# Kernel tuning notes

Hardware: AMD Instinct MI355X
Metric: run time of the kernel (lower is better)

Reference implementation:

```python
import jax, jax.numpy as jnp
import numpy as np

T, B, D_IN, D_H = 256, 256, 1024, 1024


def setup_inputs() -> dict:
    key = jax.random.key(0)
    k1, k2 = jax.random.split(key)
    seq = jax.random.normal(k1, (T, B, D_IN), dtype=jnp.float32)
    # Kaiming-ish init so tanh does not saturate
    W = jax.random.normal(k2, (D_H, D_IN + D_H), dtype=jnp.float32) / np.sqrt(D_IN + D_H)
    b = jnp.zeros((D_H,), dtype=jnp.float32)
    return {"seq": seq, "W": W, "b": b}


def reference(seq, W, b):
    # seq: (T, B, d_in); W: (d_h, d_in + d_h); b: (d_h,)
    d_h = W.shape[0]
    h0 = jnp.zeros((seq.shape[1], d_h), dtype=seq.dtype)

    def step(h, x):
        # h_{t+1} = tanh(W [h_t ; x_t] + b)
        h_new = jnp.tanh(jnp.concatenate([h, x], axis=-1) @ W.T + b)
        return h_new, h_new

    _, hs = jax.lax.scan(step, h0, seq)  # hs: (T, B, d_h)
    # Original returns the full hidden-state history including the initial zero state
    return jnp.concatenate([h0[None], hs], axis=0)  # (T+1, B, d_h)
```

## Files before the change

kernel.cpp:

```cpp
#include <hip/hip_runtime.h>

#define T_STEPS 256
#define BATCH   256
#define DIN     1024
#define DH      1024

typedef _Float16 half8_t __attribute__((ext_vector_type(8)));
typedef _Float16 half4_t __attribute__((ext_vector_type(4)));
typedef float    f32x4_t __attribute__((ext_vector_type(4)));

#define LDH  1032
#define LGW  72
#define LDS_BYTES 36864

#define CPOL_SYS 17

union H4U { half4_t h; unsigned long long u; };
union HU  { _Float16 h; unsigned short u; };

__device__ __forceinline__ float ftanh(float x) {
    float t = x * 2.885390081777927f;
    float e = exp2f(t);
    float r = __builtin_amdgcn_rcpf(e + 1.0f);
    return 1.0f - 2.0f * r;
}

__global__ __launch_bounds__(256) void cvt_w(const float* __restrict__ W,
                                             _Float16* __restrict__ Wh,
                                             _Float16* __restrict__ Wx) {
    const int part = blockIdx.x >> 9;
    size_t base = ((size_t)(blockIdx.x & 511) * 256 + threadIdx.x) * 8;
    const int n = (int)(base >> 10);
    const int k = (int)(base & 1023);
    const float4* s = reinterpret_cast<const float4*>(W + (size_t)n * 2048 + part * 1024 + k);
    float4 a = s[0], b = s[1];
    half8_t h;
    h[0] = (_Float16)a.x; h[1] = (_Float16)a.y;
    h[2] = (_Float16)a.z; h[3] = (_Float16)a.w;
    h[4] = (_Float16)b.x; h[5] = (_Float16)b.y;
    h[6] = (_Float16)b.z; h[7] = (_Float16)b.w;
    _Float16* dst = part ? Wx : Wh;
    *reinterpret_cast<half8_t*>(dst + base) = h;
}

__global__ __launch_bounds__(256) void zero_h0(float* __restrict__ out,
                                               int* __restrict__ flags,
                                               int* __restrict__ zrdy) {
    size_t i = (size_t)blockIdx.x * 256 + threadIdx.x;
    reinterpret_cast<float4*>(out)[i] = make_float4(0.f, 0.f, 0.f, 0.f);
    if (blockIdx.x == 0) {
#pragma unroll
        for (int j = 0; j < 16; ++j)
            __hip_atomic_store(&flags[(int)threadIdx.x * 16 + j], 0,
                               __ATOMIC_RELAXED, __HIP_MEMORY_SCOPE_SYSTEM);
    } else if (blockIdx.x == 1) {
#pragma unroll
        for (int j = 0; j < 16; ++j)
            __hip_atomic_store(&zrdy[(int)threadIdx.x * 16 + j], 0,
                               __ATOMIC_RELAXED, __HIP_MEMORY_SCOPE_SYSTEM);
    }
}

__global__ __launch_bounds__(256, 1) void fused_pipeline(
        const _Float16* __restrict__ Wh,
        const _Float16* __restrict__ Wx,
        const float* __restrict__ bias,
        const float* __restrict__ seq,
        _Float16* __restrict__ Hh,
        int* __restrict__ flags,
        int* __restrict__ zrdy,
        float* __restrict__ out) {
    __shared__ __align__(16) char ldsraw[LDS_BYTES];
    const int tid = threadIdx.x;
    const int bid = blockIdx.x;

    const int wave = tid >> 6;
    const int lane = tid & 63;
    const int fr   = lane & 15;
    const int quad = lane >> 4;

    if (bid >= 256) {
        _Float16* la = reinterpret_cast<_Float16*>(ldsraw);
        _Float16* lb = la + 128 * LGW;

        const int id   = bid - 256;
        const int nblk = (id >> 3) & 7;
        const int mblk = (id & 7) + 8 * (id >> 6);
        const int m0 = mblk * 128;
        const int n0 = nblk * 128;

        const float* __restrict__ X = seq + (size_t)m0 * 1024;
        float* __restrict__ Z = out + (size_t)BATCH * DH + (size_t)m0 * 1024 + n0;

        const int ar = tid >> 1;
        const int kh = tid & 1;
        const float*    Asrc = X  + (size_t)ar * 1024 + kh * 32;
        const _Float16* Bsrc = Wx + (size_t)(n0 + ar) * 1024 + kh * 32;

        float4 af[8];
        uint4  bq[4];
        auto load_tiles = [&](int kb) {
            const float4* s4 = reinterpret_cast<const float4*>(Asrc + kb);
#pragma unroll
            for (int i = 0; i < 8; ++i) af[i] = s4[i];
            const uint4* sb = reinterpret_cast<const uint4*>(Bsrc + kb);
#pragma unroll
            for (int i = 0; i < 4; ++i) bq[i] = sb[i];
        };
        auto store_tiles = [&]() {
#pragma unroll
            for (int j = 0; j < 4; ++j) {
                half8_t h;
                h[0] = (_Float16)af[2 * j].x;     h[1] = (_Float16)af[2 * j].y;
                h[2] = (_Float16)af[2 * j].z;     h[3] = (_Float16)af[2 * j].w;
                h[4] = (_Float16)af[2 * j + 1].x; h[5] = (_Float16)af[2 * j + 1].y;
                h[6] = (_Float16)af[2 * j + 1].z; h[7] = (_Float16)af[2 * j + 1].w;
                *reinterpret_cast<half8_t*>(&la[ar * LGW + kh * 32 + j * 8]) = h;
            }
#pragma unroll
            for (int i = 0; i < 4; ++i)
                *reinterpret_cast<uint4*>(&lb[ar * LGW + kh * 32 + i * 8]) = bq[i];
        };

        const int wm = (wave >> 1) * 64;
        const int wn = (wave & 1) * 64;

        f32x4_t acc[4][4];
#pragma unroll
        for (int i = 0; i < 4; ++i)
#pragma unroll
            for (int j = 0; j < 4; ++j) acc[i][j] = (f32x4_t){0.f, 0.f, 0.f, 0.f};

        load_tiles(0);
#pragma unroll 1
        for (int it = 0; it < 16; ++it) {
            store_tiles();
            __syncthreads();
            if (it < 15) load_tiles((it + 1) * 64);
#pragma unroll
            for (int kk = 0; kk < 2; ++kk) {
                const int ko = kk * 32 + quad * 8;
                half8_t a[4], b[4];
#pragma unroll
                for (int mi = 0; mi < 4; ++mi)
                    a[mi] = *reinterpret_cast<const half8_t*>(
                        &la[(wm + mi * 16 + fr) * LGW + ko]);
#pragma unroll
                for (int ni = 0; ni < 4; ++ni)
                    b[ni] = *reinterpret_cast<const half8_t*>(
                        &lb[(wn + ni * 16 + fr) * LGW + ko]);
#pragma unroll
                for (int mi = 0; mi < 4; ++mi)
#pragma unroll
                    for (int ni = 0; ni < 4; ++ni)
                        acc[mi][ni] = __builtin_amdgcn_mfma_f32_16x16x32_f16(
                            a[mi], b[ni], acc[mi][ni], 0, 0, 0);
            }
            __syncthreads();
        }

        {
            float* S = reinterpret_cast<float*>(ldsraw) + wave * (16 * 20);
#pragma unroll
            for (int ni = 0; ni < 4; ++ni) {
                const float bv = bias[n0 + wn + ni * 16 + fr];
#pragma unroll
                for (int mi = 0; mi < 4; ++mi) {
#pragma unroll
                    for (int q = 0; q < 4; ++q)
                        S[(quad * 4 + q) * 20 + fr] = acc[mi][ni][q] + bv;
                    f32x4_t t = *reinterpret_cast<const f32x4_t*>(
                        &S[fr * 20 + quad * 4]);
                    float* dst = &Z[(size_t)(wm + mi * 16 + fr) * 1024
                                    + wn + ni * 16 + quad * 4];
                    asm volatile("global_store_dwordx4 %0, %1, off sc0 sc1"
                                 :: "v"(dst), "v"(t) : "memory");
                }
            }
        }
        asm volatile("s_waitcnt vmcnt(0)" ::: "memory");
        __syncthreads();
        if (tid == 0)
            __hip_atomic_store(&zrdy[mblk * 8 + nblk], 1,
                               __ATOMIC_RELAXED, __HIP_MEMORY_SCOPE_SYSTEM);
        return;
    }

    _Float16* hL = reinterpret_cast<_Float16*>(ldsraw);

    const int m = bid & 15;
    const int n = bid >> 4;

    half8_t bfrag[32];
    {
        const _Float16* wp = Wh + (size_t)(n * 64 + wave * 16 + fr) * DH + quad * 8;
#pragma unroll
        for (int ks = 0; ks < 32; ++ks)
            bfrag[ks] = *reinterpret_cast<const half8_t*>(wp + ks * 32);
    }

    const int r  = tid >> 4;
    const int c4 = (tid & 15) * 4;
    int* myflag = flags + (m * 16 + n) * 16;
    const int zcol  = n >> 1;
    const int mhalf = m >> 3;

    const int ecol = n * 64 + wave * 16 + fr;
    const int erow0 = m * 16 + quad * 4;

    {
        if (tid == 0) {
            const int* zf = zrdy + (0 + mhalf) * 8 + zcol;
            int g = 0;
            while (!__hip_atomic_load(zf, __ATOMIC_RELAXED,
                                      __HIP_MEMORY_SCOPE_SYSTEM)) {
                if (++g > (1 << 25)) break;
            }
        }
        __syncthreads();

        float* o1 = out + ((size_t)BATCH + (size_t)(m * 16 + r)) * DH + n * 64 + c4;
        float zv[4];
#pragma unroll
        for (int j = 0; j < 4; ++j)
            zv[j] = __hip_atomic_load(o1 + j, __ATOMIC_RELAXED,
                                      __HIP_MEMORY_SCOPE_SYSTEM);
        float4 v = make_float4(ftanh(zv[0]), ftanh(zv[1]),
                               ftanh(zv[2]), ftanh(zv[3]));
        *reinterpret_cast<float4*>(o1) = v;
        H4U cv;
        cv.h[0] = (_Float16)v.x; cv.h[1] = (_Float16)v.y;
        cv.h[2] = (_Float16)v.z; cv.h[3] = (_Float16)v.w;
        __hip_atomic_store(
            (unsigned long long*)(Hh + ((size_t)BATCH + (size_t)(m * 16 + r)) * DH
                                  + n * 64 + c4),
            cv.u, __ATOMIC_RELAXED, __HIP_MEMORY_SCOPE_SYSTEM);
        __syncthreads();
        if (tid == 0)
            __hip_atomic_store(myflag, 1, __ATOMIC_RELAXED, __HIP_MEMORY_SCOPE_SYSTEM);
    }

    for (int s = 1; s < T_STEPS; ++s) {
        if (tid < 16) {
            const int* f = flags + (m * 16 + tid) * 16;
            int guard = 0;
            while (__hip_atomic_load(f, __ATOMIC_RELAXED,
                                     __HIP_MEMORY_SCOPE_SYSTEM) < s) {
                if (++guard > (1 << 25)) break;
            }
        } else if (tid == 16) {
            const int* zf = zrdy + (2 * s + mhalf) * 8 + zcol;
            int guard = 0;
            while (!__hip_atomic_load(zf, __ATOMIC_RELAXED,
                                      __HIP_MEMORY_SCOPE_SYSTEM)) {
                if (++guard > (1 << 25)) break;
            }
        }
        __syncthreads();

        const _Float16* hsrc = Hh + ((size_t)(s & 1) * BATCH + (size_t)m * 16) * DH;
#pragma unroll
        for (int i = 0; i < 8; ++i) {
            const int c   = wave * 8 + i;
            const int row = c >> 1;
            const int hf  = c & 1;
            const _Float16* src = hsrc + (size_t)row * DH + hf * 512 + lane * 8;
            __builtin_amdgcn_global_load_lds(
                (const __attribute__((address_space(1))) void*)src,
                (__attribute__((address_space(3))) void*)&hL[row * LDH + hf * 512],
                16, 0, CPOL_SYS);
        }
        float zv[4];
#pragma unroll
        for (int q = 0; q < 4; ++q)
            zv[q] = __hip_atomic_load(
                out + ((size_t)(s + 1) * BATCH + erow0 + q) * DH + ecol,
                __ATOMIC_RELAXED, __HIP_MEMORY_SCOPE_SYSTEM);
        __syncthreads();

        f32x4_t acc0 = {0.f, 0.f, 0.f, 0.f}, acc1 = {0.f, 0.f, 0.f, 0.f};
        const _Float16* pa = &hL[fr * LDH + quad * 8];
#pragma unroll
        for (int ks = 0; ks < 16; ++ks) {
            half8_t ae = *reinterpret_cast<const half8_t*>(pa + (2 * ks) * 32);
            half8_t ao = *reinterpret_cast<const half8_t*>(pa + (2 * ks + 1) * 32);
            acc0 = __builtin_amdgcn_mfma_f32_16x16x32_f16(ae, bfrag[2 * ks],     acc0, 0, 0, 0);
            acc1 = __builtin_amdgcn_mfma_f32_16x16x32_f16(ao, bfrag[2 * ks + 1], acc1, 0, 0, 0);
        }
        f32x4_t sum = acc0 + acc1;

#pragma unroll
        for (int q = 0; q < 4; ++q) {
            const float v = ftanh(sum[q] + zv[q]);
            *(out + ((size_t)(s + 1) * BATCH + erow0 + q) * DH + ecol) = v;
            HU hu; hu.h = (_Float16)v;
            __hip_atomic_store(
                (unsigned short*)(Hh + ((size_t)((s + 1) & 1) * BATCH + erow0 + q) * DH
                                  + ecol),
                hu.u, __ATOMIC_RELAXED, __HIP_MEMORY_SCOPE_SYSTEM);
        }

        __syncthreads();
        if (tid == 0)
            __hip_atomic_store(myflag, s + 1, __ATOMIC_RELAXED, __HIP_MEMORY_SCOPE_SYSTEM);
    }
}

extern "C" void kernel_launch(void* const* d_in, const int* in_sizes, int n_in,
                              void* d_out, int out_size, void* d_ws, size_t ws_size,
                              hipStream_t stream) {
    const float* seq  = (const float*)d_in[0];
    const float* W    = (const float*)d_in[1];
    const float* bias = (const float*)d_in[2];
    float* out        = (float*)d_out;
    _Float16* Wh      = (_Float16*)d_ws;
    _Float16* Wx      = (_Float16*)d_ws + 1024 * 1024;
    _Float16* Hh      = (_Float16*)d_ws + 2 * 1024 * 1024;
    int* flags        = (int*)((char*)d_ws + 5 * 1024 * 1024);
    int* zrdy         = (int*)((char*)d_ws + 5 * 1024 * 1024 + 16 * 1024);

    hipLaunchKernelGGL(cvt_w, dim3(1024), dim3(256), 0, stream, W, Wh, Wx);
    hipLaunchKernelGGL(zero_h0, dim3(256), dim3(256), 0, stream, out, flags, zrdy);
    hipLaunchKernelGGL(fused_pipeline, dim3(256 + 4096), dim3(256), 0, stream,
                       Wh, Wx, bias, seq, Hh, flags, zrdy, out);
}
```

Baseline: 1.342 ms.

## Halve recurrent blocks by giving each block 128 hidden columns

The recurrent part now uses 128 persistent blocks instead of 256. Each wave computes two 16-column output fragments and keeps twice as many Wh fragments in registers. Each block waits on 8 peer flags instead of 16, which cuts the per-step cross-block synchronisation fan-in and frees compute units for the input-projection GEMM blocks. The cost is a doubled register footprint (64 half8 fragments per lane, which risks spills) and twice the MFMA work per block on the serial critical path.

```diff
diff --git a/kernel.cpp b/kernel.cpp
--- a/kernel.cpp
+++ b/kernel.cpp
@@ -79,11 +79,11 @@
     const int fr   = lane & 15;
     const int quad = lane >> 4;
 
-    if (bid >= 256) {
+    if (bid >= 128) {
         _Float16* la = reinterpret_cast<_Float16*>(ldsraw);
         _Float16* lb = la + 128 * LGW;
 
-        const int id   = bid - 256;
+        const int id   = bid - 128;
         const int nblk = (id >> 3) & 7;
         const int mblk = (id & 7) + 8 * (id >> 6);
         const int m0 = mblk * 128;
@@ -191,26 +191,28 @@
     const int m = bid & 15;
     const int n = bid >> 4;
 
-    half8_t bfrag[32];
-    {
-        const _Float16* wp = Wh + (size_t)(n * 64 + wave * 16 + fr) * DH + quad * 8;
+    half8_t bfrag[2][32];
+#pragma unroll
+    for (int cf = 0; cf < 2; ++cf) {
+        const _Float16* wp = Wh + (size_t)(n * 128 + wave * 32 + cf * 16 + fr) * DH
+                                + quad * 8;
 #pragma unroll
         for (int ks = 0; ks < 32; ++ks)
-            bfrag[ks] = *reinterpret_cast<const half8_t*>(wp + ks * 32);
+            bfrag[cf][ks] = *reinterpret_cast<const half8_t*>(wp + ks * 32);
     }
 
     const int r  = tid >> 4;
     const int c4 = (tid & 15) * 4;
-    int* myflag = flags + (m * 16 + n) * 16;
-    const int zcol  = n >> 1;
+    int* myflag = flags + (m * 8 + n) * 16;
     const int mhalf = m >> 3;
 
-    const int ecol = n * 64 + wave * 16 + fr;
+    const int ecol0 = n * 128 + wave * 32 + fr;
+    const int ecol1 = ecol0 + 16;
     const int erow0 = m * 16 + quad * 4;
 
     {
         if (tid == 0) {
-            const int* zf = zrdy + (0 + mhalf) * 8 + zcol;
+            const int* zf = zrdy + mhalf * 8 + n;
             int g = 0;
             while (!__hip_atomic_load(zf, __ATOMIC_RELAXED,
                                       __HIP_MEMORY_SCOPE_SYSTEM)) {
@@ -219,37 +221,41 @@
         }
         __syncthreads();
 
-        float* o1 = out + ((size_t)BATCH + (size_t)(m * 16 + r)) * DH + n * 64 + c4;
-        float zv[4];
-#pragma unroll
-        for (int j = 0; j < 4; ++j)
-            zv[j] = __hip_atomic_load(o1 + j, __ATOMIC_RELAXED,
-                                      __HIP_MEMORY_SCOPE_SYSTEM);
-        float4 v = make_float4(ftanh(zv[0]), ftanh(zv[1]),
-                               ftanh(zv[2]), ftanh(zv[3]));
-        *reinterpret_cast<float4*>(o1) = v;
-        H4U cv;
-        cv.h[0] = (_Float16)v.x; cv.h[1] = (_Float16)v.y;
-        cv.h[2] = (_Float16)v.z; cv.h[3] = (_Float16)v.w;
-        __hip_atomic_store(
-            (unsigned long long*)(Hh + ((size_t)BATCH + (size_t)(m * 16 + r)) * DH
-                                  + n * 64 + c4),
-            cv.u, __ATOMIC_RELAXED, __HIP_MEMORY_SCOPE_SYSTEM);
+#pragma unroll
+        for (int cc = 0; cc < 128; cc += 64) {
+            float* o1 = out + ((size_t)BATCH + (size_t)(m * 16 + r)) * DH
+                            + n * 128 + cc + c4;
+            float zv[4];
+#pragma unroll
+            for (int j = 0; j < 4; ++j)
+                zv[j] = __hip_atomic_load(o1 + j, __ATOMIC_RELAXED,
+                                          __HIP_MEMORY_SCOPE_SYSTEM);
+            float4 v = make_float4(ftanh(zv[0]), ftanh(zv[1]),
+                                   ftanh(zv[2]), ftanh(zv[3]));
+            *reinterpret_cast<float4*>(o1) = v;
+            H4U cv;
+            cv.h[0] = (_Float16)v.x; cv.h[1] = (_Float16)v.y;
+            cv.h[2] = (_Float16)v.z; cv.h[3] = (_Float16)v.w;
+            __hip_atomic_store(
+                (unsigned long long*)(Hh + ((size_t)BATCH + (size_t)(m * 16 + r)) * DH
+                                      + n * 128 + cc + c4),
+                cv.u, __ATOMIC_RELAXED, __HIP_MEMORY_SCOPE_SYSTEM);
+        }
         __syncthreads();
         if (tid == 0)
             __hip_atomic_store(myflag, 1, __ATOMIC_RELAXED, __HIP_MEMORY_SCOPE_SYSTEM);
     }
 
     for (int s = 1; s < T_STEPS; ++s) {
-        if (tid < 16) {
-            const int* f = flags + (m * 16 + tid) * 16;
+        if (tid < 8) {
+            const int* f = flags + (m * 8 + tid) * 16;
             int guard = 0;
             while (__hip_atomic_load(f, __ATOMIC_RELAXED,
                                      __HIP_MEMORY_SCOPE_SYSTEM) < s) {
                 if (++guard > (1 << 25)) break;
             }
-        } else if (tid == 16) {
-            const int* zf = zrdy + (2 * s + mhalf) * 8 + zcol;
+        } else if (tid == 8) {
+            const int* zf = zrdy + (2 * s + mhalf) * 8 + n;
             int guard = 0;
             while (!__hip_atomic_load(zf, __ATOMIC_RELAXED,
                                       __HIP_MEMORY_SCOPE_SYSTEM)) {
@@ -270,34 +276,46 @@
                 (__attribute__((address_space(3))) void*)&hL[row * LDH + hf * 512],
                 16, 0, CPOL_SYS);
         }
-        float zv[4];
-#pragma unroll
-        for (int q = 0; q < 4; ++q)
-            zv[q] = __hip_atomic_load(
-                out + ((size_t)(s + 1) * BATCH + erow0 + q) * DH + ecol,
-                __ATOMIC_RELAXED, __HIP_MEMORY_SCOPE_SYSTEM);
-        __syncthreads();
-
-        f32x4_t acc0 = {0.f, 0.f, 0.f, 0.f}, acc1 = {0.f, 0.f, 0.f, 0.f};
+        float zv0[4], zv1[4];
+#pragma unroll
+        for (int q = 0; q < 4; ++q) {
+            const float* zb = out + ((size_t)(s + 1) * BATCH + erow0 + q) * DH;
+            zv0[q] = __hip_atomic_load(zb + ecol0, __ATOMIC_RELAXED,
+                                       __HIP_MEMORY_SCOPE_SYSTEM);
+            zv1[q] = __hip_atomic_load(zb + ecol1, __ATOMIC_RELAXED,
+                                       __HIP_MEMORY_SCOPE_SYSTEM);
+        }
+        __syncthreads();
+
+        f32x4_t a00 = {0.f,0.f,0.f,0.f}, a01 = {0.f,0.f,0.f,0.f};
+        f32x4_t a10 = {0.f,0.f,0.f,0.f}, a11 = {0.f,0.f,0.f,0.f};
         const _Float16* pa = &hL[fr * LDH + quad * 8];
 #pragma unroll
         for (int ks = 0; ks < 16; ++ks) {
             half8_t ae = *reinterpret_cast<const half8_t*>(pa + (2 * ks) * 32);
             half8_t ao = *reinterpret_cast<const half8_t*>(pa + (2 * ks + 1) * 32);
-            acc0 = __builtin_amdgcn_mfma_f32_16x16x32_f16(ae, bfrag[2 * ks],     acc0, 0, 0, 0);
-            acc1 = __builtin_amdgcn_mfma_f32_16x16x32_f16(ao, bfrag[2 * ks + 1], acc1, 0, 0, 0);
-        }
-        f32x4_t sum = acc0 + acc1;
+            a00 = __builtin_amdgcn_mfma_f32_16x16x32_f16(ae, bfrag[0][2 * ks],     a00, 0, 0, 0);
+            a01 = __builtin_amdgcn_mfma_f32_16x16x32_f16(ao, bfrag[0][2 * ks + 1], a01, 0, 0, 0);
+            a10 = __builtin_amdgcn_mfma_f32_16x16x32_f16(ae, bfrag[1][2 * ks],     a10, 0, 0, 0);
+            a11 = __builtin_amdgcn_mfma_f32_16x16x32_f16(ao, bfrag[1][2 * ks + 1], a11, 0, 0, 0);
+        }
+        f32x4_t sum0 = a00 + a01;
+        f32x4_t sum1 = a10 + a11;
 
 #pragma unroll
         for (int q = 0; q < 4; ++q) {
-            const float v = ftanh(sum[q] + zv[q]);
-            *(out + ((size_t)(s + 1) * BATCH + erow0 + q) * DH + ecol) = v;
-            HU hu; hu.h = (_Float16)v;
-            __hip_atomic_store(
-                (unsigned short*)(Hh + ((size_t)((s + 1) & 1) * BATCH + erow0 + q) * DH
-                                  + ecol),
-                hu.u, __ATOMIC_RELAXED, __HIP_MEMORY_SCOPE_SYSTEM);
+            float* ob = out + ((size_t)(s + 1) * BATCH + erow0 + q) * DH;
+            _Float16* hb = Hh + ((size_t)((s + 1) & 1) * BATCH + erow0 + q) * DH;
+            const float v0 = ftanh(sum0[q] + zv0[q]);
+            const float v1 = ftanh(sum1[q] + zv1[q]);
+            ob[ecol0] = v0;
+            ob[ecol1] = v1;
+            HU h0; h0.h = (_Float16)v0;
+            HU h1; h1.h = (_Float16)v1;
+            __hip_atomic_store((unsigned short*)(hb + ecol0), h0.u,
+                               __ATOMIC_RELAXED, __HIP_MEMORY_SCOPE_SYSTEM);
+            __hip_atomic_store((unsigned short*)(hb + ecol1), h1.u,
+                               __ATOMIC_RELAXED, __HIP_MEMORY_SCOPE_SYSTEM);
         }
 
         __syncthreads();
@@ -321,6 +339,6 @@
 
     hipLaunchKernelGGL(cvt_w, dim3(1024), dim3(256), 0, stream, W, Wh, Wx);
     hipLaunchKernelGGL(zero_h0, dim3(256), dim3(256), 0, stream, out, flags, zrdy);
-    hipLaunchKernelGGL(fused_pipeline, dim3(256 + 4096), dim3(256), 0, stream,
+    hipLaunchKernelGGL(fused_pipeline, dim3(128 + 4096), dim3(256), 0, stream,
                        Wh, Wx, bias, seq, Hh, flags, zrdy, out);
 }
```

After: 1.826 ms. +36.1%, slower.
